# Performance work log

Hardware: AMD Instinct MI355X
Metric: run time of the kernel (lower is better)

Reference implementation:

```python
import jax, jax.numpy as jnp
import numpy as np

N_NODES = 100000
N_EDGES = 3200000
IN_F, HID_F, OUT_F = 128, 128, 64
BN_EPS = 1e-5


def setup_inputs() -> dict:
    key = jax.random.key(0)
    ks = jax.random.split(key, 12)
    x = jax.random.normal(ks[0], (N_NODES, IN_F), dtype=jnp.float32)
    src = jax.random.randint(ks[1], (N_EDGES,), 0, N_NODES, dtype=jnp.int64)
    dst = jax.random.randint(ks[2], (N_EDGES,), 0, N_NODES, dtype=jnp.int64)
    s = 0.05
    W1 = jax.random.normal(ks[3], (IN_F, HID_F), dtype=jnp.float32) * s
    b1 = jnp.zeros((HID_F,), jnp.float32)
    W2 = jax.random.normal(ks[4], (HID_F, HID_F), dtype=jnp.float32) * s
    b2 = jnp.zeros((HID_F,), jnp.float32)
    W3 = jax.random.normal(ks[5], (HID_F, OUT_F), dtype=jnp.float32) * s
    b3 = jnp.zeros((OUT_F,), jnp.float32)
    gamma1 = jnp.ones((HID_F,), jnp.float32)
    beta1 = jnp.zeros((HID_F,), jnp.float32)
    gamma2 = jnp.ones((HID_F,), jnp.float32)
    beta2 = jnp.zeros((HID_F,), jnp.float32)
    return {"x": x, "src": src, "dst": dst,
            "W1": W1, "b1": b1, "W2": W2, "b2": b2, "W3": W3, "b3": b3,
            "gamma1": gamma1, "beta1": beta1, "gamma2": gamma2, "beta2": beta2}


def reference(x, src, dst, W1, b1, W2, b2, W3, b3, gamma1, beta1, gamma2, beta2):
    n = x.shape[0]
    ones = jnp.ones((src.shape[0],), x.dtype)
    # DGL GraphConv(norm='both'): symmetric normalization, degrees clamped to >=1
    deg_out = jax.ops.segment_sum(ones, src, num_segments=n)
    deg_in = jax.ops.segment_sum(ones, dst, num_segments=n)
    norm_s = jax.lax.rsqrt(jnp.maximum(deg_out, 1.0))[:, None]
    norm_d = jax.lax.rsqrt(jnp.maximum(deg_in, 1.0))[:, None]

    def conv(h, W, b):
        h = h * norm_s                                   # [N, F] scale by out-deg^{-1/2}
        m = jax.ops.segment_sum(h[src], dst, num_segments=n)  # SpMM aggregation
        return (m * norm_d) @ W + b

    def bn(h, g, b):  # BatchNorm1d, training-mode batch stats (biased var)
        mu = jnp.mean(h, axis=0)
        var = jnp.var(h, axis=0)
        return (h - mu) * jax.lax.rsqrt(var + BN_EPS) * g + b

    h = bn(jax.nn.relu(conv(x, W1, b1)), gamma1, beta1)
    h = bn(jax.nn.relu(conv(h, W2, b2)), gamma2, beta2)
    h = conv(h, W3, b3)
    return jax.nn.log_softmax(h, axis=1)
```

## Files before the change

### kernel.cpp

```cpp
#include <hip/hip_runtime.h>
#include <hip/hip_bf16.h>
#include <cstdint>

static constexpr int N = 100000;
static constexpr int E = 3200000;
static constexpr float BN_EPS = 1e-5f;
static constexpr int NBUCK = (N + 127) >> 7;
static constexpr int NBLK = 256;
static constexpr int CHUNK = E / NBLK;
static constexpr int AGG_BLOCKS = 2048;
static constexpr int NWAVE = AGG_BLOCKS * 4;

static constexpr size_t OFF_TOT_D = 0;
static constexpr size_t OFF_TOT_S = 3328;
static constexpr size_t OFF_DBASE = 6656;
static constexpr size_t OFF_SBASE = 9984;
static constexpr size_t OFF_CVEC  = 15360;
static constexpr size_t OFF_WT    = 16384;
static constexpr size_t OFF_WSRT  = 49152;
static constexpr size_t OFF_BNP2  = 82944;
static constexpr size_t OFF_BNP   = 148480;
static constexpr size_t OFF_NORM_S= 2245632;
static constexpr size_t OFF_NORM_D= 2645632;
static constexpr size_t OFF_RP    = 3045632;
static constexpr size_t OFF_CNT_D = 3445760;
static constexpr size_t OFF_CNT_S = 4246528;
static constexpr size_t OFF_OFFD  = 5047296;
static constexpr size_t OFF_OFFS  = 5848064;
static constexpr size_t OFF_COL   = 6648832;
static constexpr size_t OFF_SRCB  = 19448832;
static constexpr size_t OFF_PAIRS = 22648832;
static constexpr size_t OFF_H     = 35448832;
static constexpr size_t OFF_T     = 61048832;

using short8  = __attribute__((ext_vector_type(8))) short;
using float4v = __attribute__((ext_vector_type(4))) float;

__device__ inline float bflo(unsigned v) { return __uint_as_float(v << 16); }
__device__ inline float bfhi(unsigned v) { return __uint_as_float(v & 0xffff0000u); }
__device__ inline unsigned short bfbits(float x) {
    __hip_bfloat16 h = __float2bfloat16(x);
    return *reinterpret_cast<unsigned short*>(&h);
}

__global__ __launch_bounds__(256) void k_count(const int* __restrict__ src,
                                               const int* __restrict__ dst,
                                               int* __restrict__ cnt_s,
                                               int* __restrict__ cnt_d) {
    __shared__ int hs[NBUCK], hd[NBUCK];
    int tid = threadIdx.x, blk = blockIdx.x;
    for (int b = tid; b < NBUCK; b += 256) { hs[b] = 0; hd[b] = 0; }
    __syncthreads();
    int e0 = blk * CHUNK, e1 = min(E, e0 + CHUNK);
    for (int e = e0 + tid; e < e1; e += 256) {
        atomicAdd(&hs[src[e] >> 7], 1);
        atomicAdd(&hd[dst[e] >> 7], 1);
    }
    __syncthreads();
    for (int b = tid; b < NBUCK; b += 256) {
        cnt_s[blk * NBUCK + b] = hs[b];
        cnt_d[blk * NBUCK + b] = hd[b];
    }
}

__global__ __launch_bounds__(256) void k_scanA2(const int* __restrict__ cnt_d,
                                                const int* __restrict__ cnt_s,
                                                int* __restrict__ offd,
                                                int* __restrict__ offs,
                                                int* __restrict__ tot_d,
                                                int* __restrict__ tot_s) {
    __shared__ int sd[256];
    int which = (blockIdx.x >= NBUCK) ? 1 : 0;
    int b = blockIdx.x - which * NBUCK;
    const int* cnt = which ? cnt_s : cnt_d;
    int* off = which ? offs : offd;
    int* tot = which ? tot_s : tot_d;
    int tid = threadIdx.x;
    int v = cnt[tid * NBUCK + b];
    sd[tid] = v;
    __syncthreads();
    for (int o = 1; o < 256; o <<= 1) {
        int t = (tid >= o) ? sd[tid - o] : 0;
        __syncthreads();
        sd[tid] += t;
        __syncthreads();
    }
    off[tid * NBUCK + b] = sd[tid] - v;
    if (tid == 255) tot[b] = sd[255];
}

__global__ __launch_bounds__(1024) void k_scanB(const int* __restrict__ tot_d,
                                                const int* __restrict__ tot_s,
                                                int* __restrict__ dbase,
                                                int* __restrict__ sbase) {
    __shared__ int sd[1024], ss[1024];
    int tid = threadIdx.x;
    int vd = (tid < NBUCK) ? tot_d[tid] : 0;
    int vs = (tid < NBUCK) ? tot_s[tid] : 0;
    sd[tid] = vd; ss[tid] = vs;
    __syncthreads();
    for (int o = 1; o < 1024; o <<= 1) {
        int td = (tid >= o) ? sd[tid - o] : 0;
        int ts = (tid >= o) ? ss[tid - o] : 0;
        __syncthreads();
        sd[tid] += td; ss[tid] += ts;
        __syncthreads();
    }
    if (tid < NBUCK) { dbase[tid] = sd[tid] - vd; sbase[tid] = ss[tid] - vs; }
    if (tid == 0) { dbase[NBUCK] = E; sbase[NBUCK] = E; }
}

__global__ __launch_bounds__(256) void k_scatter(const int* __restrict__ src,
                                                 const int* __restrict__ dst,
                                                 const int* __restrict__ dbase,
                                                 const int* __restrict__ sbase,
                                                 const int* __restrict__ offd,
                                                 const int* __restrict__ offs,
                                                 unsigned* __restrict__ pairs,
                                                 unsigned char* __restrict__ srcb) {
    __shared__ int cd[NBUCK], cs[NBUCK];
    int tid = threadIdx.x, blk = blockIdx.x;
    for (int b = tid; b < NBUCK; b += 256) {
        cd[b] = dbase[b] + offd[blk * NBUCK + b];
        cs[b] = sbase[b] + offs[blk * NBUCK + b];
    }
    __syncthreads();
    int e0 = blk * CHUNK, e1 = min(E, e0 + CHUNK);
    for (int e = e0 + tid; e < e1; e += 256) {
        int s = src[e], d = dst[e];
        int pd = atomicAdd(&cd[d >> 7], 1);
        pairs[pd] = (unsigned)s | ((unsigned)(d & 127) << 20);
        int ps = atomicAdd(&cs[s >> 7], 1);
        srcb[ps] = (unsigned char)(s & 127);
    }
}

__global__ __launch_bounds__(256) void k_build(const unsigned* __restrict__ pairs,
                                               const unsigned char* __restrict__ srcb,
                                               const int* __restrict__ dbase,
                                               const int* __restrict__ sbase,
                                               int* __restrict__ rp,
                                               float* __restrict__ norm_d,
                                               float* __restrict__ norm_s,
                                               int* __restrict__ col) {
    __shared__ int cnt[128], scn[128], lcur[128];
    int b = blockIdx.x, tid = threadIdx.x, node0 = b << 7;
    int nmax = min(128, N - node0);
    if (tid < 128) cnt[tid] = 0;
    __syncthreads();
    int sb = sbase[b], se = sbase[b + 1];
    for (int e = sb + tid; e < se; e += 256) atomicAdd(&cnt[srcb[e]], 1);
    __syncthreads();
    if (tid < nmax) norm_s[node0 + tid] = rsqrtf(fmaxf((float)cnt[tid], 1.0f));
    __syncthreads();
    if (tid < 128) cnt[tid] = 0;
    __syncthreads();
    int beg = dbase[b], end = dbase[b + 1];
    for (int e = beg + tid; e < end; e += 256) atomicAdd(&cnt[pairs[e] >> 20], 1);
    __syncthreads();
    if (tid < 128) scn[tid] = cnt[tid];
    __syncthreads();
    for (int o = 1; o < 128; o <<= 1) {
        int t = (tid < 128 && tid >= o) ? scn[tid - o] : 0;
        __syncthreads();
        if (tid < 128) scn[tid] += t;
        __syncthreads();
    }
    if (tid < nmax) {
        int excl = beg + scn[tid] - cnt[tid];
        rp[node0 + tid] = excl;
        lcur[tid] = excl;
        norm_d[node0 + tid] = rsqrtf(fmaxf((float)cnt[tid], 1.0f));
    }
    if (b == 0 && tid == 0) rp[N] = E;
    __syncthreads();
    for (int e = beg + tid; e < end; e += 256) {
        unsigned p = pairs[e];
        int pos = atomicAdd(&lcur[p >> 20], 1);
        col[pos] = (int)(p & 0xFFFFFu);
    }
}

__global__ __launch_bounds__(256) void k_wpart(const int* __restrict__ rp,
                                               int* __restrict__ wsrt) {
    int w = blockIdx.x * 256 + threadIdx.x;
    if (w > NWAVE) return;
    if (w == 0) { wsrt[0] = 0; return; }
    if (w == NWAVE) { wsrt[NWAVE] = N; return; }
    int t = (int)((long long)w * E / NWAVE);
    int lo = 0, hi = N;
    while (lo < hi) { int mid = (lo + hi) >> 1; if (rp[mid] >= t) hi = mid; else lo = mid + 1; }
    wsrt[w] = lo;
}

template <bool AFFINE>
__global__ __launch_bounds__(64) void k_wprep(const float* __restrict__ W,
                                              const float* __restrict__ part2,
                                              const float* __restrict__ gamma,
                                              const float* __restrict__ beta,
                                              int fout,
                                              unsigned short* __restrict__ Wt,
                                              float* __restrict__ cvec) {
    int n = blockIdx.x, k = threadIdx.x;
    float a0 = 1.f, c0 = 0.f, a1 = 1.f, c1 = 0.f;
    if (AFFINE) {
        int l0 = ((k & 1) ? 128 : 0) + (k >> 1);
        int m0 = ((k & 1) ? 192 : 64) + (k >> 1);
        int l1 = l0 + 32, m1 = m0 + 32;
        float s0 = 0.f, q0 = 0.f, s1 = 0.f, q1 = 0.f;
        for (int b = 0; b < 64; ++b) {
            const float* r = part2 + b * 256;
            s0 += r[l0]; q0 += r[m0];
            s1 += r[l1]; q1 += r[m1];
        }
        float mu0 = s0 * (1.0f / N), var0 = q0 * (1.0f / N) - mu0 * mu0;
        a0 = gamma[k] * rsqrtf(var0 + BN_EPS);
        c0 = beta[k] - mu0 * a0;
        float mu1 = s1 * (1.0f / N), var1 = q1 * (1.0f / N) - mu1 * mu1;
        a1 = gamma[k + 64] * rsqrtf(var1 + BN_EPS);
        c1 = beta[k + 64] - mu1 * a1;
    }
    float w0 = W[k * fout + n], w1 = W[(k + 64) * fout + n];
    Wt[n * 128 + k] = bfbits(a0 * w0);
    Wt[n * 128 + k + 64] = bfbits(a1 * w1);
    float cv = c0 * w0 + c1 * w1;
    for (int o = 32; o; o >>= 1) cv += __shfl_xor(cv, o);
    if (k == 0) cvec[n] = cv;
}

template <typename TIn, int FOUT>
__global__ __launch_bounds__(256) void k_gemm(const TIn* __restrict__ in,
                                              const unsigned short* __restrict__ Wt,
                                              const float* __restrict__ cvec,
                                              const float* __restrict__ ns,
                                              unsigned short* __restrict__ out) {
    constexpr int PK = 72;
    __shared__ __align__(16) unsigned short Xs[128 * PK];
    __shared__ __align__(16) unsigned short Wsh[FOUT * PK];
    const int tid = threadIdx.x;
    const int r0 = blockIdx.x * 128;
    const int wave = tid >> 6, lane = tid & 63;
    const int l16 = lane & 15, quad = lane >> 4;
    constexpr int MT = (FOUT == 128) ? 4 : 2;
    constexpr int NT = 4;
    const int wm = (FOUT == 128) ? (wave >> 1) : wave;
    const int wn = (FOUT == 128) ? (wave & 1) : 0;
    const int mbase = wm * (MT * 16);
    const int nbase = wn * 64;

    float4v acc[MT][NT];
#pragma unroll
    for (int mt = 0; mt < MT; ++mt)
#pragma unroll
        for (int nt = 0; nt < NT; ++nt) acc[mt][nt] = (float4v){0.f, 0.f, 0.f, 0.f};

    for (int kb = 0; kb < 128; kb += 64) {
        __syncthreads();
        for (int i = tid; i < 128 * 8; i += 256) {
            int row = i >> 3, j = i & 7;
            int grow = r0 + row;
            if constexpr (sizeof(TIn) == 4) {
                short8 p = {0, 0, 0, 0, 0, 0, 0, 0};
                if (grow < N) {
                    const float* g = (const float*)in + (size_t)grow * 128 + kb + j * 8;
                    float4 f0 = *(const float4*)g;
                    float4 f1 = *(const float4*)(g + 4);
                    p[0] = (short)bfbits(f0.x); p[1] = (short)bfbits(f0.y);
                    p[2] = (short)bfbits(f0.z); p[3] = (short)bfbits(f0.w);
                    p[4] = (short)bfbits(f1.x); p[5] = (short)bfbits(f1.y);
                    p[6] = (short)bfbits(f1.z); p[7] = (short)bfbits(f1.w);
                }
                *(short8*)&Xs[row * PK + j * 8] = p;
            } else {
                uint4 v = make_uint4(0, 0, 0, 0);
                if (grow < N)
                    v = *(const uint4*)((const unsigned short*)in + (size_t)grow * 128 + kb + j * 8);
                *(uint4*)&Xs[row * PK + j * 8] = v;
            }
        }
        for (int i = tid; i < FOUT * 8; i += 256) {
            int n = i >> 3, j = i & 7;
            uint4 v = *(const uint4*)&Wt[n * 128 + kb + j * 8];
            *(uint4*)&Wsh[n * PK + j * 8] = v;
        }
        __syncthreads();
#pragma unroll
        for (int ks = 0; ks < 64; ks += 32) {
            short8 af[MT], bfr[NT];
#pragma unroll
            for (int mt = 0; mt < MT; ++mt)
                af[mt] = *(const short8*)&Xs[(mbase + mt * 16 + l16) * PK + ks + quad * 8];
#pragma unroll
            for (int nt = 0; nt < NT; ++nt)
                bfr[nt] = *(const short8*)&Wsh[(nbase + nt * 16 + l16) * PK + ks + quad * 8];
#pragma unroll
            for (int mt = 0; mt < MT; ++mt)
#pragma unroll
                for (int nt = 0; nt < NT; ++nt)
                    acc[mt][nt] = __builtin_amdgcn_mfma_f32_16x16x32_bf16(
                        af[mt], bfr[nt], acc[mt][nt], 0, 0, 0);
        }
    }
    float cv[NT];
#pragma unroll
    for (int nt = 0; nt < NT; ++nt) cv[nt] = cvec[nbase + nt * 16 + l16];
#pragma unroll
    for (int mt = 0; mt < MT; ++mt) {
#pragma unroll
        for (int r = 0; r < 4; ++r) {
            int row = r0 + mbase + mt * 16 + quad * 4 + r;
            if (row < N) {
                float s = ns[row];
#pragma unroll
                for (int nt = 0; nt < NT; ++nt)
                    out[(size_t)row * FOUT + nbase + nt * 16 + l16] =
                        bfbits((acc[mt][nt][r] + cv[nt]) * s);
            }
        }
    }
}

__global__ __launch_bounds__(256, 8) void k_agg128f(const unsigned* __restrict__ T2,
                                                    const int* __restrict__ wsrt,
                                                    const int* __restrict__ rp,
                                                    const int* __restrict__ col,
                                                    const float* __restrict__ norm_d,
                                                    const float* __restrict__ bias,
                                                    unsigned* __restrict__ Hu,
                                                    float* __restrict__ part) {
    int tid = threadIdx.x, wave = tid >> 6, lane = tid & 63;
    int w = blockIdx.x * 4 + wave;
    int n0 = wsrt[w], n1 = wsrt[w + 1];
    float bb0 = bias[2 * lane], bb1 = bias[2 * lane + 1];
    float s0 = 0.f, q0 = 0.f, s1 = 0.f, q1 = 0.f;
    for (int n = n0; n < n1; ++n) {
        int beg = rp[n], end = rp[n + 1];
        float a0 = 0.0f, a1 = 0.0f;
        int e = beg;
        for (; e + 16 <= end; e += 16) {
            int c[16];
#pragma unroll
            for (int i = 0; i < 16; ++i) c[i] = col[e + i];
            unsigned v[16];
#pragma unroll
            for (int i = 0; i < 16; ++i) v[i] = T2[(size_t)c[i] * 64 + lane];
#pragma unroll
            for (int i = 0; i < 16; ++i) { a0 += bflo(v[i]); a1 += bfhi(v[i]); }
        }
        for (; e + 8 <= end; e += 8) {
            int c[8];
#pragma unroll
            for (int i = 0; i < 8; ++i) c[i] = col[e + i];
            unsigned v[8];
#pragma unroll
            for (int i = 0; i < 8; ++i) v[i] = T2[(size_t)c[i] * 64 + lane];
#pragma unroll
            for (int i = 0; i < 8; ++i) { a0 += bflo(v[i]); a1 += bfhi(v[i]); }
        }
        for (; e < end; ++e) {
            unsigned v = T2[(size_t)col[e] * 64 + lane];
            a0 += bflo(v); a1 += bfhi(v);
        }
        float nd = norm_d[n];
        float r0 = fmaxf(a0 * nd + bb0, 0.0f);
        float r1 = fmaxf(a1 * nd + bb1, 0.0f);
        Hu[(size_t)n * 64 + lane] = ((unsigned)bfbits(r1) << 16) | bfbits(r0);
        s0 += r0; q0 += r0 * r0; s1 += r1; q1 += r1 * r1;
    }
    __shared__ float red[4][256];
    red[wave][lane] = s0;
    red[wave][64 + lane] = q0;
    red[wave][128 + lane] = s1;
    red[wave][192 + lane] = q1;
    __syncthreads();
    float t = red[0][tid] + red[1][tid] + red[2][tid] + red[3][tid];
    part[blockIdx.x * 256 + tid] = t;
}

__global__ __launch_bounds__(256) void k_bnred(const float* __restrict__ part,
                                               float* __restrict__ part2) {
    int b = blockIdx.x, tid = threadIdx.x;
    float s = 0.f;
    for (int i = 0; i < AGG_BLOCKS / 64; ++i)
        s += part[(b * (AGG_BLOCKS / 64) + i) * 256 + tid];
    part2[b * 256 + tid] = s;
}

__global__ __launch_bounds__(256, 8) void k_agg64f(const __hip_bfloat16* __restrict__ T,
                                                   const int* __restrict__ wsrt,
                                                   const int* __restrict__ rp,
                                                   const int* __restrict__ col,
                                                   const float* __restrict__ norm_d,
                                                   const float* __restrict__ b3,
                                                   float* __restrict__ out) {
    int wave = threadIdx.x >> 6, lane = threadIdx.x & 63;
    int w = blockIdx.x * 4 + wave;
    int n0 = wsrt[w], n1 = wsrt[w + 1];
    float bb = b3[lane];
    for (int n = n0; n < n1; ++n) {
        int beg = rp[n], end = rp[n + 1];
        float a0 = 0.0f;
        int e = beg;
        for (; e + 16 <= end; e += 16) {
            int c[16];
#pragma unroll
            for (int i = 0; i < 16; ++i) c[i] = col[e + i];
            float v[16];
#pragma unroll
            for (int i = 0; i < 16; ++i) v[i] = __bfloat162float(T[(size_t)c[i] * 64 + lane]);
#pragma unroll
            for (int i = 0; i < 16; ++i) a0 += v[i];
        }
        for (; e + 8 <= end; e += 8) {
            int c[8];
#pragma unroll
            for (int i = 0; i < 8; ++i) c[i] = col[e + i];
            float v[8];
#pragma unroll
            for (int i = 0; i < 8; ++i) v[i] = __bfloat162float(T[(size_t)c[i] * 64 + lane]);
#pragma unroll
            for (int i = 0; i < 8; ++i) a0 += v[i];
        }
        for (; e < end; ++e) a0 += __bfloat162float(T[(size_t)col[e] * 64 + lane]);
        float z = a0 * norm_d[n] + bb;
        float m = z;
        for (int o = 32; o; o >>= 1) m = fmaxf(m, __shfl_xor(m, o));
        float ex = __expf(z - m);
        float ssum = ex;
        for (int o = 32; o; o >>= 1) ssum += __shfl_xor(ssum, o);
        out[(size_t)n * 64 + lane] = z - m - __logf(ssum);
    }
}

extern "C" void kernel_launch(void* const* d_in, const int* in_sizes, int n_in,
                              void* d_out, int out_size, void* d_ws, size_t ws_size,
                              hipStream_t stream) {
    const float* x  = (const float*)d_in[0];
    const int* src  = (const int*)d_in[1];
    const int* dst  = (const int*)d_in[2];
    const float* W1 = (const float*)d_in[3];
    const float* b1 = (const float*)d_in[4];
    const float* W2 = (const float*)d_in[5];
    const float* b2 = (const float*)d_in[6];
    const float* W3 = (const float*)d_in[7];
    const float* b3 = (const float*)d_in[8];
    const float* g1 = (const float*)d_in[9];
    const float* be1= (const float*)d_in[10];
    const float* g2 = (const float*)d_in[11];
    const float* be2= (const float*)d_in[12];
    float* out = (float*)d_out;

    char* ws = (char*)d_ws;
    int* tot_d = (int*)(ws + OFF_TOT_D);
    int* tot_s = (int*)(ws + OFF_TOT_S);
    int* dbase = (int*)(ws + OFF_DBASE);
    int* sbase = (int*)(ws + OFF_SBASE);
    float* cvec = (float*)(ws + OFF_CVEC);
    unsigned short* Wt = (unsigned short*)(ws + OFF_WT);
    int* wsrt = (int*)(ws + OFF_WSRT);
    float* bnp2 = (float*)(ws + OFF_BNP2);
    float* bnp = (float*)(ws + OFF_BNP);
    float* norm_s = (float*)(ws + OFF_NORM_S);
    float* norm_d = (float*)(ws + OFF_NORM_D);
    int* rp = (int*)(ws + OFF_RP);
    int* cnt_d = (int*)(ws + OFF_CNT_D);
    int* cnt_s = (int*)(ws + OFF_CNT_S);
    int* offd = (int*)(ws + OFF_OFFD);
    int* offs = (int*)(ws + OFF_OFFS);
    int* col = (int*)(ws + OFF_COL);
    unsigned char* srcb = (unsigned char*)(ws + OFF_SRCB);
    unsigned* pairs = (unsigned*)(ws + OFF_PAIRS);
    unsigned short* H = (unsigned short*)(ws + OFF_H);
    unsigned short* T = (unsigned short*)(ws + OFF_T);

    k_count<<<NBLK, 256, 0, stream>>>(src, dst, cnt_s, cnt_d);
    k_scanA2<<<2 * NBUCK, 256, 0, stream>>>(cnt_d, cnt_s, offd, offs, tot_d, tot_s);
    k_scanB<<<1, 1024, 0, stream>>>(tot_d, tot_s, dbase, sbase);
    k_scatter<<<NBLK, 256, 0, stream>>>(src, dst, dbase, sbase, offd, offs, pairs, srcb);
    k_build<<<NBUCK, 256, 0, stream>>>(pairs, srcb, dbase, sbase, rp, norm_d, norm_s, col);
    k_wpart<<<(NWAVE + 256) / 256, 256, 0, stream>>>(rp, wsrt);

    const int gemm_grid = (N + 127) / 128;

    k_wprep<false><<<128, 64, 0, stream>>>(W1, nullptr, nullptr, nullptr, 128, Wt, cvec);
    k_gemm<float, 128><<<gemm_grid, 256, 0, stream>>>(x, Wt, cvec, norm_s, T);
    k_agg128f<<<AGG_BLOCKS, 256, 0, stream>>>((const unsigned*)T, wsrt, rp, col, norm_d, b1, (unsigned*)H, bnp);
    k_bnred<<<64, 256, 0, stream>>>(bnp, bnp2);

    k_wprep<true><<<128, 64, 0, stream>>>(W2, bnp2, g1, be1, 128, Wt, cvec);
    k_gemm<__hip_bfloat16, 128><<<gemm_grid, 256, 0, stream>>>((const __hip_bfloat16*)H, Wt, cvec, norm_s, T);
    k_agg128f<<<AGG_BLOCKS, 256, 0, stream>>>((const unsigned*)T, wsrt, rp, col, norm_d, b2, (unsigned*)H, bnp);
    k_bnred<<<64, 256, 0, stream>>>(bnp, bnp2);

    k_wprep<true><<<64, 64, 0, stream>>>(W3, bnp2, g2, be2, 64, Wt, cvec);
    k_gemm<__hip_bfloat16, 64><<<gemm_grid, 256, 0, stream>>>((const __hip_bfloat16*)H, Wt, cvec, norm_s, T);
    k_agg64f<<<AGG_BLOCKS, 256, 0, stream>>>((const __hip_bfloat16*)T, wsrt, rp, col, norm_d, b3, out);
}
```

Before: 647.9 us.

## Reorder edges per 16-node group by source slice for gather locality

A new preprocessing kernel replaces the edge-balanced wave partition. It assigns each wave a fixed group of 16 destination nodes and reorders that group's edges by source-node slice (8192-node buckets). Each edge is packed with its local destination index. The aggregation kernels accumulate partial sums per destination in shared memory, so gathers within a wave sweep source rows in address order and should get better cache locality. The cost is an extra preprocessing pass and shared-memory read-modify-writes whenever the destination changes, plus lower occupancy and possible load imbalance from the fixed node partition.

```diff
diff --git a/kernel.cpp b/kernel.cpp
--- a/kernel.cpp
+++ b/kernel.cpp
@@ -8,8 +8,12 @@
 static constexpr int NBUCK = (N + 127) >> 7;
 static constexpr int NBLK = 256;
 static constexpr int CHUNK = E / NBLK;
-static constexpr int AGG_BLOCKS = 2048;
-static constexpr int NWAVE = AGG_BLOCKS * 4;
+
+static constexpr int NW2 = N / 16;
+static constexpr int AGG2_BLOCKS = (NW2 + 3) / 4;
+static constexpr int NSLICE = ((N - 1) >> 13) + 1;
+static constexpr int NBKT = NSLICE * 16;
+static constexpr int BNRED_PER = (AGG2_BLOCKS + 63) / 64;
 
 static constexpr size_t OFF_TOT_D = 0;
 static constexpr size_t OFF_TOT_S = 3328;
@@ -17,7 +21,6 @@
 static constexpr size_t OFF_SBASE = 9984;
 static constexpr size_t OFF_CVEC  = 15360;
 static constexpr size_t OFF_WT    = 16384;
-static constexpr size_t OFF_WSRT  = 49152;
 static constexpr size_t OFF_BNP2  = 82944;
 static constexpr size_t OFF_BNP   = 148480;
 static constexpr size_t OFF_NORM_S= 2245632;
@@ -181,16 +184,38 @@
     }
 }
 
-__global__ __launch_bounds__(256) void k_wpart(const int* __restrict__ rp,
-                                               int* __restrict__ wsrt) {
-    int w = blockIdx.x * 256 + threadIdx.x;
-    if (w > NWAVE) return;
-    if (w == 0) { wsrt[0] = 0; return; }
-    if (w == NWAVE) { wsrt[NWAVE] = N; return; }
-    int t = (int)((long long)w * E / NWAVE);
-    int lo = 0, hi = N;
-    while (lo < hi) { int mid = (lo + hi) >> 1; if (rp[mid] >= t) hi = mid; else lo = mid + 1; }
-    wsrt[w] = lo;
+__global__ __launch_bounds__(256) void k_eprep(const int* __restrict__ col,
+                                               const int* __restrict__ rp,
+                                               unsigned* __restrict__ epk) {
+    __shared__ int cnt[4][NBKT];
+    int tid = threadIdx.x, wave = tid >> 6, lane = tid & 63;
+    int w = blockIdx.x * 4 + wave;
+    bool val = (w < NW2);
+    for (int k = lane; k < NBKT; k += 64) cnt[wave][k] = 0;
+    int rpl[17];
+    int n0 = (w < NW2 ? w : 0) << 4;
+#pragma unroll
+    for (int j = 0; j <= 16; ++j) rpl[j] = rp[n0 + j];
+    __syncthreads();
+    if (val) {
+        for (int j = 0; j < 16; ++j)
+            for (int e = rpl[j] + lane; e < rpl[j + 1]; e += 64)
+                atomicAdd(&cnt[wave][(((unsigned)col[e]) >> 13) * 16 + j], 1);
+    }
+    __syncthreads();
+    if (val && lane == 0) {
+        int run = rpl[0];
+        for (int k = 0; k < NBKT; ++k) { int c = cnt[wave][k]; cnt[wave][k] = run; run += c; }
+    }
+    __syncthreads();
+    if (val) {
+        for (int j = 0; j < 16; ++j)
+            for (int e = rpl[j] + lane; e < rpl[j + 1]; e += 64) {
+                unsigned c = (unsigned)col[e];
+                int pos = atomicAdd(&cnt[wave][(c >> 13) * 16 + j], 1);
+                epk[pos] = c | ((unsigned)j << 17);
+            }
+    }
 }
 
 template <bool AFFINE>
@@ -320,54 +345,75 @@
     }
 }
 
-__global__ __launch_bounds__(256, 8) void k_agg128f(const unsigned* __restrict__ T2,
-                                                    const int* __restrict__ wsrt,
+__global__ __launch_bounds__(256, 4) void k_agg128s(const unsigned* __restrict__ T2,
                                                     const int* __restrict__ rp,
-                                                    const int* __restrict__ col,
+                                                    const unsigned* __restrict__ epk,
                                                     const float* __restrict__ norm_d,
                                                     const float* __restrict__ bias,
                                                     unsigned* __restrict__ Hu,
                                                     float* __restrict__ part) {
-    int tid = threadIdx.x, wave = tid >> 6, lane = tid & 63;
-    int w = blockIdx.x * 4 + wave;
-    int n0 = wsrt[w], n1 = wsrt[w + 1];
-    float bb0 = bias[2 * lane], bb1 = bias[2 * lane + 1];
+    __shared__ __align__(16) float acc[4][16][128];
+    __shared__ float red[4][256];
+    const int tid = threadIdx.x, wave = tid >> 6, lane = tid & 63;
+    const int w = blockIdx.x * 4 + wave;
+    float2* accw = (float2*)&acc[wave][0][0];
+#pragma unroll
+    for (int j = 0; j < 16; ++j) accw[j * 64 + lane] = make_float2(0.f, 0.f);
     float s0 = 0.f, q0 = 0.f, s1 = 0.f, q1 = 0.f;
-    for (int n = n0; n < n1; ++n) {
-        int beg = rp[n], end = rp[n + 1];
-        float a0 = 0.0f, a1 = 0.0f;
-        int e = beg;
-        for (; e + 16 <= end; e += 16) {
-            int c[16];
-#pragma unroll
-            for (int i = 0; i < 16; ++i) c[i] = col[e + i];
+    if (w < NW2) {
+        const int n0 = w << 4;
+        int e = rp[n0];
+        const int e1 = rp[n0 + 16];
+        int cur = 0;
+        float a0 = 0.f, a1 = 0.f;
+        for (; e + 16 <= e1; e += 16) {
+            unsigned p[16];
+#pragma unroll
+            for (int i = 0; i < 16; ++i) p[i] = epk[e + i];
             unsigned v[16];
 #pragma unroll
-            for (int i = 0; i < 16; ++i) v[i] = T2[(size_t)c[i] * 64 + lane];
-#pragma unroll
-            for (int i = 0; i < 16; ++i) { a0 += bflo(v[i]); a1 += bfhi(v[i]); }
-        }
-        for (; e + 8 <= end; e += 8) {
-            int c[8];
-#pragma unroll
-            for (int i = 0; i < 8; ++i) c[i] = col[e + i];
-            unsigned v[8];
-#pragma unroll
-            for (int i = 0; i < 8; ++i) v[i] = T2[(size_t)c[i] * 64 + lane];
-#pragma unroll
-            for (int i = 0; i < 8; ++i) { a0 += bflo(v[i]); a1 += bfhi(v[i]); }
-        }
-        for (; e < end; ++e) {
-            unsigned v = T2[(size_t)col[e] * 64 + lane];
+            for (int i = 0; i < 16; ++i) v[i] = T2[(size_t)(p[i] & 0x1FFFFu) * 64 + lane];
+#pragma unroll
+            for (int i = 0; i < 16; ++i) {
+                int dl = __builtin_amdgcn_readfirstlane((int)(p[i] >> 17));
+                if (dl != cur) {
+                    float2 t = accw[cur * 64 + lane];
+                    t.x += a0; t.y += a1;
+                    accw[cur * 64 + lane] = t;
+                    cur = dl; a0 = 0.f; a1 = 0.f;
+                }
+                a0 += bflo(v[i]); a1 += bfhi(v[i]);
+            }
+        }
+        for (; e < e1; ++e) {
+            unsigned p = epk[e];
+            unsigned v = T2[(size_t)(p & 0x1FFFFu) * 64 + lane];
+            int dl = __builtin_amdgcn_readfirstlane((int)(p >> 17));
+            if (dl != cur) {
+                float2 t = accw[cur * 64 + lane];
+                t.x += a0; t.y += a1;
+                accw[cur * 64 + lane] = t;
+                cur = dl; a0 = 0.f; a1 = 0.f;
+            }
             a0 += bflo(v); a1 += bfhi(v);
         }
-        float nd = norm_d[n];
-        float r0 = fmaxf(a0 * nd + bb0, 0.0f);
-        float r1 = fmaxf(a1 * nd + bb1, 0.0f);
-        Hu[(size_t)n * 64 + lane] = ((unsigned)bfbits(r1) << 16) | bfbits(r0);
-        s0 += r0; q0 += r0 * r0; s1 += r1; q1 += r1 * r1;
-    }
-    __shared__ float red[4][256];
+        {
+            float2 t = accw[cur * 64 + lane];
+            t.x += a0; t.y += a1;
+            accw[cur * 64 + lane] = t;
+        }
+        const float bb0 = bias[2 * lane], bb1 = bias[2 * lane + 1];
+#pragma unroll
+        for (int j = 0; j < 16; ++j) {
+            int n = n0 + j;
+            float2 a = accw[j * 64 + lane];
+            float nd = norm_d[n];
+            float r0 = fmaxf(a.x * nd + bb0, 0.0f);
+            float r1 = fmaxf(a.y * nd + bb1, 0.0f);
+            Hu[(size_t)n * 64 + lane] = ((unsigned)bfbits(r1) << 16) | bfbits(r0);
+            s0 += r0; q0 += r0 * r0; s1 += r1; q1 += r1 * r1;
+        }
+    }
     red[wave][lane] = s0;
     red[wave][64 + lane] = q0;
     red[wave][128 + lane] = s1;
@@ -381,48 +427,65 @@
                                                float* __restrict__ part2) {
     int b = blockIdx.x, tid = threadIdx.x;
     float s = 0.f;
-    for (int i = 0; i < AGG_BLOCKS / 64; ++i)
-        s += part[(b * (AGG_BLOCKS / 64) + i) * 256 + tid];
+    for (int i = 0; i < BNRED_PER; ++i) {
+        int r = b * BNRED_PER + i;
+        if (r < AGG2_BLOCKS) s += part[r * 256 + tid];
+    }
     part2[b * 256 + tid] = s;
 }
 
-__global__ __launch_bounds__(256, 8) void k_agg64f(const __hip_bfloat16* __restrict__ T,
-                                                   const int* __restrict__ wsrt,
+__global__ __launch_bounds__(256, 4) void k_agg64s(const __hip_bfloat16* __restrict__ T,
                                                    const int* __restrict__ rp,
-                                                   const int* __restrict__ col,
+                                                   const unsigned* __restrict__ epk,
                                                    const float* __restrict__ norm_d,
                                                    const float* __restrict__ b3,
                                                    float* __restrict__ out) {
-    int wave = threadIdx.x >> 6, lane = threadIdx.x & 63;
-    int w = blockIdx.x * 4 + wave;
-    int n0 = wsrt[w], n1 = wsrt[w + 1];
-    float bb = b3[lane];
-    for (int n = n0; n < n1; ++n) {
-        int beg = rp[n], end = rp[n + 1];
-        float a0 = 0.0f;
-        int e = beg;
-        for (; e + 16 <= end; e += 16) {
-            int c[16];
-#pragma unroll
-            for (int i = 0; i < 16; ++i) c[i] = col[e + i];
-            float v[16];
-#pragma unroll
-            for (int i = 0; i < 16; ++i) v[i] = __bfloat162float(T[(size_t)c[i] * 64 + lane]);
-#pragma unroll
-            for (int i = 0; i < 16; ++i) a0 += v[i];
-        }
-        for (; e + 8 <= end; e += 8) {
-            int c[8];
-#pragma unroll
-            for (int i = 0; i < 8; ++i) c[i] = col[e + i];
-            float v[8];
-#pragma unroll
-            for (int i = 0; i < 8; ++i) v[i] = __bfloat162float(T[(size_t)c[i] * 64 + lane]);
-#pragma unroll
-            for (int i = 0; i < 8; ++i) a0 += v[i];
-        }
-        for (; e < end; ++e) a0 += __bfloat162float(T[(size_t)col[e] * 64 + lane]);
-        float z = a0 * norm_d[n] + bb;
+    __shared__ float acc[4][16][64];
+    const int tid = threadIdx.x, wave = tid >> 6, lane = tid & 63;
+    const int w = blockIdx.x * 4 + wave;
+    if (w >= NW2) return;
+    float* accw = &acc[wave][0][0];
+#pragma unroll
+    for (int j = 0; j < 16; ++j) accw[j * 64 + lane] = 0.f;
+    const int n0 = w << 4;
+    int e = rp[n0];
+    const int e1 = rp[n0 + 16];
+    int cur = 0;
+    float a0 = 0.f;
+    for (; e + 16 <= e1; e += 16) {
+        unsigned p[16];
+#pragma unroll
+        for (int i = 0; i < 16; ++i) p[i] = epk[e + i];
+        float v[16];
+#pragma unroll
+        for (int i = 0; i < 16; ++i)
+            v[i] = __bfloat162float(T[(size_t)(p[i] & 0x1FFFFu) * 64 + lane]);
+#pragma unroll
+        for (int i = 0; i < 16; ++i) {
+            int dl = __builtin_amdgcn_readfirstlane((int)(p[i] >> 17));
+            if (dl != cur) {
+                accw[cur * 64 + lane] += a0;
+                cur = dl; a0 = 0.f;
+            }
+            a0 += v[i];
+        }
+    }
+    for (; e < e1; ++e) {
+        unsigned p = epk[e];
+        float v = __bfloat162float(T[(size_t)(p & 0x1FFFFu) * 64 + lane]);
+        int dl = __builtin_amdgcn_readfirstlane((int)(p >> 17));
+        if (dl != cur) {
+            accw[cur * 64 + lane] += a0;
+            cur = dl; a0 = 0.f;
+        }
+        a0 += v;
+    }
+    accw[cur * 64 + lane] += a0;
+    const float bb = b3[lane];
+#pragma unroll
+    for (int j = 0; j < 16; ++j) {
+        int n = n0 + j;
+        float z = accw[j * 64 + lane] * norm_d[n] + bb;
         float m = z;
         for (int o = 32; o; o >>= 1) m = fmaxf(m, __shfl_xor(m, o));
         float ex = __expf(z - m);
@@ -457,7 +520,6 @@
     int* sbase = (int*)(ws + OFF_SBASE);
     float* cvec = (float*)(ws + OFF_CVEC);
     unsigned short* Wt = (unsigned short*)(ws + OFF_WT);
-    int* wsrt = (int*)(ws + OFF_WSRT);
     float* bnp2 = (float*)(ws + OFF_BNP2);
     float* bnp = (float*)(ws + OFF_BNP);
     float* norm_s = (float*)(ws + OFF_NORM_S);
@@ -470,6 +532,7 @@
     int* col = (int*)(ws + OFF_COL);
     unsigned char* srcb = (unsigned char*)(ws + OFF_SRCB);
     unsigned* pairs = (unsigned*)(ws + OFF_PAIRS);
+    unsigned* epk = pairs;
     unsigned short* H = (unsigned short*)(ws + OFF_H);
     unsigned short* T = (unsigned short*)(ws + OFF_T);
 
@@ -478,21 +541,21 @@
     k_scanB<<<1, 1024, 0, stream>>>(tot_d, tot_s, dbase, sbase);
     k_scatter<<<NBLK, 256, 0, stream>>>(src, dst, dbase, sbase, offd, offs, pairs, srcb);
     k_build<<<NBUCK, 256, 0, stream>>>(pairs, srcb, dbase, sbase, rp, norm_d, norm_s, col);
-    k_wpart<<<(NWAVE + 256) / 256, 256, 0, stream>>>(rp, wsrt);
+    k_eprep<<<AGG2_BLOCKS, 256, 0, stream>>>(col, rp, epk);
 
     const int gemm_grid = (N + 127) / 128;
 
     k_wprep<false><<<128, 64, 0, stream>>>(W1, nullptr, nullptr, nullptr, 128, Wt, cvec);
     k_gemm<float, 128><<<gemm_grid, 256, 0, stream>>>(x, Wt, cvec, norm_s, T);
-    k_agg128f<<<AGG_BLOCKS, 256, 0, stream>>>((const unsigned*)T, wsrt, rp, col, norm_d, b1, (unsigned*)H, bnp);
+    k_agg128s<<<AGG2_BLOCKS, 256, 0, stream>>>((const unsigned*)T, rp, epk, norm_d, b1, (unsigned*)H, bnp);
     k_bnred<<<64, 256, 0, stream>>>(bnp, bnp2);
 
     k_wprep<true><<<128, 64, 0, stream>>>(W2, bnp2, g1, be1, 128, Wt, cvec);
     k_gemm<__hip_bfloat16, 128><<<gemm_grid, 256, 0, stream>>>((const __hip_bfloat16*)H, Wt, cvec, norm_s, T);
-    k_agg128f<<<AGG_BLOCKS, 256, 0, stream>>>((const unsigned*)T, wsrt, rp, col, norm_d, b2, (unsigned*)H, bnp);
+    k_agg128s<<<AGG2_BLOCKS, 256, 0, stream>>>((const unsigned*)T, rp, epk, norm_d, b2, (unsigned*)H, bnp);
     k_bnred<<<64, 256, 0, stream>>>(bnp, bnp2);
 
     k_wprep<true><<<64, 64, 0, stream>>>(W3, bnp2, g2, be2, 64, Wt, cvec);
     k_gemm<__hip_bfloat16, 64><<<gemm_grid, 256, 0, stream>>>((const __hip_bfloat16*)H, Wt, cvec, norm_s, T);
-    k_agg64f<<<AGG_BLOCKS, 256, 0, stream>>>((const __hip_bfloat16*)T, wsrt, rp, col, norm_d, b3, out);
-}
+    k_agg64s<<<AGG2_BLOCKS, 256, 0, stream>>>((const __hip_bfloat16*)T, rp, epk, norm_d, b3, out);
+}
```

Measured after the change: 659.6 us. No clear change (+1.8%).
